# Kernel tuning notes

Hardware: AMD Instinct MI355X
Metric: run time of the kernel (lower is better)

Reference implementation:

```python
import jax, jax.numpy as jnp
import numpy as np

B, D, NTXT, H = 16384, 512, 4096, 1024


def _linear_params(key, fan_in, fan_out):
    kw, kb = jax.random.split(key)
    s = 1.0 / np.sqrt(fan_in)
    W = jax.random.uniform(kw, (fan_in, fan_out), jnp.float32, -s, s)
    b = jax.random.uniform(kb, (fan_out,), jnp.float32, -s, s)
    return W, b


def setup_inputs() -> dict:
    key = jax.random.key(0)
    ks = jax.random.split(key, 9)
    img_features = jax.random.normal(ks[0], (B, D), jnp.float32)
    txt_features = jax.random.normal(ks[1], (D, NTXT), jnp.float32)
    target_ind = jax.random.randint(ks[2], (B,), 0, NTXT, jnp.int32)
    Wi0, bi0 = _linear_params(ks[3], D, H)
    Wi1, bi1 = _linear_params(ks[4], H, H)
    Wi2, bi2 = _linear_params(ks[5], H, D)
    Wt0, bt0 = _linear_params(ks[6], D, H)
    Wt1, bt1 = _linear_params(ks[7], H, H)
    Wt2, bt2 = _linear_params(ks[8], H, D)
    logit_scale = jnp.asarray(np.log(1.0 / 0.07), jnp.float32)
    temp = jnp.asarray(1.0, jnp.float32)
    return {
        "img_features": img_features, "txt_features": txt_features,
        "target_ind": target_ind, "temp": temp,
        "Wi0": Wi0, "bi0": bi0, "Wi1": Wi1, "bi1": bi1, "Wi2": Wi2, "bi2": bi2,
        "Wt0": Wt0, "bt0": bt0, "Wt1": Wt1, "bt1": bt1, "Wt2": Wt2, "bt2": bt2,
        "logit_scale": logit_scale,
    }


def _mlp(x, params):
    # ReLU after every layer except the last (matches MLP.forward)
    for W, b in params[:-1]:
        x = jax.nn.relu(x @ W + b)
    W, b = params[-1]
    return x @ W + b


def reference(img_features, txt_features, target_ind, temp,
              Wi0, bi0, Wi1, bi1, Wi2, bi2,
              Wt0, bt0, Wt1, bt1, Wt2, bt2, logit_scale):
    p_img = _mlp(img_features, [(Wi0, bi0), (Wi1, bi1), (Wi2, bi2)])          # [B, D]
    p_txt = _mlp(txt_features.T, [(Wt0, bt0), (Wt1, bt1), (Wt2, bt2)])        # [N, D]

    sim = (p_img @ p_txt.T) * jnp.exp(logit_scale)                            # [B, N]
    sim = sim / jnp.linalg.norm(sim, axis=-1, keepdims=True)
    out_logits = sim / jnp.linalg.norm(sim, axis=-1, keepdims=True)           # faithful double-normalize

    # vectorized form of the per-sample Python-loop softmax-CE in MLP_CLIP_loss
    logp = jax.nn.log_softmax(out_logits / temp, axis=-1)                     # [B, N]
    picked = jnp.take_along_axis(logp, target_ind[:, None].astype(jnp.int32), axis=1)[:, 0]
    loss = -jnp.mean(picked)

    # accuracy branch (uses unscaled similarity, row-normalized)
    sim_clip = p_img @ p_txt.T
    sim_clip = sim_clip / jnp.linalg.norm(sim_clip, axis=-1, keepdims=True)
    acc = jnp.sum(jnp.argmax(sim_clip, axis=1).astype(jnp.int32) == target_ind)
    return loss, acc
```

## Files before the change

kernel.cpp:

```cpp
#include <hip/hip_runtime.h>
#include <cstdint>
#include <cstddef>

#define B_ROWS 16384
#define D_DIM  512
#define NTXT_N 4096
#define H_DIM  1024

typedef __attribute__((ext_vector_type(8))) short short8;
typedef __attribute__((ext_vector_type(4))) float f32x4;

__device__ __forceinline__ ushort f2bf(float x) {
    union { float f; uint32_t u; } c; c.f = x;
    const uint32_t u = c.u;
    return (ushort)((u + 0x7fffu + ((u >> 16) & 1u)) >> 16);
}
__device__ __forceinline__ float bf2f(ushort h) {
    union { uint32_t u; float f; } c; c.u = ((uint32_t)h) << 16;
    return c.f;
}

#define GLDS16(gp, lp) __builtin_amdgcn_global_load_lds( \
    (const __attribute__((address_space(1))) void*)(gp),  \
    (__attribute__((address_space(3))) void*)(lp), 16, 0, 0)

__device__ __forceinline__ void xcd_remap(int& bx, int& by) {
    const int nx = gridDim.x, ny = gridDim.y;
    const int nwg = nx * ny;
    const int bid = by * nx + bx;
    const int q = nwg >> 3, r = nwg & 7;
    const int xcd = bid & 7, idx = bid >> 3;
    const int nb = (xcd < r ? xcd * (q + 1) : r * (q + 1) + (xcd - r) * q) + idx;
    bx = nb % nx; by = nb / nx;
}

__global__ void init_kernel(int* acc) {
    if (threadIdx.x == 0 && blockIdx.x == 0) *acc = 0;
}

__global__ void tsplit_kernel(const float* __restrict__ in, ushort* __restrict__ oh,
                              ushort* __restrict__ ol, int R, int C, int cbase)
{
    __shared__ float tile[32][33];
    const int c0 = blockIdx.x * 32, r0 = blockIdx.y * 32;
    const int tx = threadIdx.x, ty = threadIdx.y;
    #pragma unroll
    for (int j = 0; j < 32; j += 8)
        tile[ty + j][tx] = in[(size_t)(r0 + ty + j) * C + cbase + c0 + tx];
    __syncthreads();
    #pragma unroll
    for (int j = 0; j < 32; j += 8) {
        const float v = tile[tx][ty + j];
        const ushort h = f2bf(v);
        const size_t idx = (size_t)(c0 + ty + j) * R + r0 + tx;
        oh[idx] = h;
        ol[idx] = f2bf(v - bf2f(h));
    }
}

__global__ void csplit_kernel(const float* __restrict__ in, ushort* __restrict__ oh,
                              ushort* __restrict__ ol, int n)
{
    const int i = (blockIdx.x * 256 + threadIdx.x) * 4;
    if (i >= n) return;
    const float4 f = *(const float4*)&in[i];
    ushort4 h, l;
    h.x = f2bf(f.x); l.x = f2bf(f.x - bf2f(h.x));
    h.y = f2bf(f.y); l.y = f2bf(f.y - bf2f(h.y));
    h.z = f2bf(f.z); l.z = f2bf(f.z - bf2f(h.z));
    h.w = f2bf(f.w); l.w = f2bf(f.w - bf2f(h.w));
    *(ushort4*)&oh[i] = h;
    *(ushort4*)&ol[i] = l;
}

template<int K, int OMODE, bool RELU, bool BIAS>
__global__ __launch_bounds__(256, 2)
void gemm_p2_kernel(const ushort* __restrict__ Ah, const ushort* __restrict__ Al,
                    const ushort* __restrict__ Bh, const ushort* __restrict__ Bl,
                    const float* __restrict__ bias,
                    float* __restrict__ Cf, ushort* __restrict__ Ch, ushort* __restrict__ Cl,
                    int M, int N)
{
    constexpr int NT = K / 32;
    __shared__ __align__(16) ushort LDSB[2 * 4 * 4096];

    const int tid  = threadIdx.x;
    const int lane = tid & 63;
    const int w    = tid >> 6;
    const int wr   = w >> 1, wc = w & 1;

    int bxi = blockIdx.x, byi = blockIdx.y;
    xcd_remap(bxi, byi);
    const int bm = byi * 128, bn = bxi * 128;

    const int    stlo  = w * 1024;
    const int    srow  = w * 32 + (lane >> 2);
    const int    scol  = (((lane & 3) ^ ((lane >> 3) & 3)) << 3);
    const size_t aoff0 = (size_t)(bm + srow) * K + scol;
    const size_t boff0 = (size_t)(bn + srow) * K + scol;

    const int frow = lane & 15;
    const int koff = ((lane >> 4) ^ ((frow >> 1) & 3)) << 3;

    f32x4 acc[4][4];
    #pragma unroll
    for (int m = 0; m < 4; ++m)
        #pragma unroll
        for (int n = 0; n < 4; ++n)
            acc[m][n] = (f32x4)0.0f;

#define STAGE(tt, bi) do {                                                    \
        const int _kk = (tt) * 32;                                            \
        ushort* _b = &LDSB[(bi) * 16384];                                     \
        GLDS16(Ah + aoff0 + _kk,          _b +         stlo);                 \
        GLDS16(Ah + aoff0 + _kk + 16 * K, _b +         stlo + 512);           \
        GLDS16(Al + aoff0 + _kk,          _b +  4096 + stlo);                 \
        GLDS16(Al + aoff0 + _kk + 16 * K, _b +  4096 + stlo + 512);           \
        GLDS16(Bh + boff0 + _kk,          _b +  8192 + stlo);                 \
        GLDS16(Bh + boff0 + _kk + 16 * K, _b +  8192 + stlo + 512);           \
        GLDS16(Bl + boff0 + _kk,          _b + 12288 + stlo);                 \
        GLDS16(Bl + boff0 + _kk + 16 * K, _b + 12288 + stlo + 512);           \
    } while (0)

#define COMPUTE(bi) do {                                                      \
        const ushort* _Ahs = &LDSB[(bi) * 16384];                             \
        const ushort* _Als = _Ahs + 4096;                                     \
        const ushort* _Bhs = _Ahs + 8192;                                     \
        const ushort* _Bls = _Ahs + 12288;                                    \
        short8 a_h[4], a_l[4], b_h[4], b_l[4];                                \
        _Pragma("unroll")                                                     \
        for (int m = 0; m < 4; ++m) {                                         \
            const int off = (wr * 64 + m * 16 + frow) * 32 + koff;            \
            a_h[m] = *(const short8*)&_Ahs[off];                              \
            a_l[m] = *(const short8*)&_Als[off];                              \
        }                                                                     \
        _Pragma("unroll")                                                     \
        for (int n = 0; n < 4; ++n) {                                         \
            const int off = (wc * 64 + n * 16 + frow) * 32 + koff;            \
            b_h[n] = *(const short8*)&_Bhs[off];                              \
            b_l[n] = *(const short8*)&_Bls[off];                              \
        }                                                                     \
        __builtin_amdgcn_s_setprio(1);                                        \
        _Pragma("unroll")                                                     \
        for (int m = 0; m < 4; ++m)                                           \
            _Pragma("unroll")                                                 \
            for (int n = 0; n < 4; ++n) {                                     \
                acc[m][n] = __builtin_amdgcn_mfma_f32_16x16x32_bf16(          \
                    a_h[m], b_h[n], acc[m][n], 0, 0, 0);                      \
                acc[m][n] = __builtin_amdgcn_mfma_f32_16x16x32_bf16(          \
                    a_h[m], b_l[n], acc[m][n], 0, 0, 0);                      \
                acc[m][n] = __builtin_amdgcn_mfma_f32_16x16x32_bf16(          \
                    a_l[m], b_h[n], acc[m][n], 0, 0, 0);                      \
            }                                                                 \
        __builtin_amdgcn_s_setprio(0);                                        \
    } while (0)

    STAGE(0, 0);
    #pragma unroll 2
    for (int t = 0; t < NT; ++t) {
        __syncthreads();
        if (t + 1 < NT) STAGE(t + 1, (t + 1) & 1);
        COMPUTE(t & 1);
    }

#undef STAGE
#undef COMPUTE

    const int crow0 = bm + wr * 64 + (lane >> 4) * 4;
    const int ccol0 = bn + wc * 64 + (lane & 15);
    #pragma unroll
    for (int m = 0; m < 4; ++m)
        #pragma unroll
        for (int n = 0; n < 4; ++n) {
            const int col = ccol0 + n * 16;
            const float bv = BIAS ? bias[col] : 0.0f;
            #pragma unroll
            for (int q = 0; q < 4; ++q) {
                float v = acc[m][n][q] + bv;
                if (RELU) v = fmaxf(v, 0.0f);
                const size_t idx = (size_t)(crow0 + m * 16 + q) * N + col;
                if (OMODE == 0) {
                    Cf[idx] = v;
                } else {
                    const ushort h = f2bf(v);
                    Ch[idx] = h;
                    Cl[idx] = f2bf(v - bf2f(h));
                }
            }
        }
}

template<int K, int OMODE, bool RELU, bool BIAS>
__global__ __launch_bounds__(512, 2)
void gemm256_kernel(const ushort* __restrict__ Ah, const ushort* __restrict__ Al,
                    const ushort* __restrict__ Bh, const ushort* __restrict__ Bl,
                    const float* __restrict__ bias,
                    float* __restrict__ Cf, ushort* __restrict__ Ch, ushort* __restrict__ Cl,
                    int M, int N)
{
    constexpr int NT = K / 32;
    __shared__ __align__(16) ushort LDSB[2 * 4 * 8192];

    const int tid  = threadIdx.x;
    const int lane = tid & 63;
    const int w    = tid >> 6;
    const int wr   = w >> 2, wc = w & 3;

    int bxi = blockIdx.x, byi = blockIdx.y;
    xcd_remap(bxi, byi);
    const int bm = byi * 256, bn = bxi * 256;

    const int    srow  = tid >> 2;
    const int    scol  = (((tid & 3) ^ ((tid >> 3) & 3)) << 3);
    const size_t aoffA = (size_t)(bm + srow) * K + scol;
    const size_t aoffB = (size_t)(bm + 128 + srow) * K + scol;
    const size_t boffA = (size_t)(bn + srow) * K + scol;
    const size_t boffB = (size_t)(bn + 128 + srow) * K + scol;
    const int    dst   = srow * 32 + (tid & 3) * 8;

    const int frow = lane & 15;
    const int koff = ((lane >> 4) ^ ((frow >> 1) & 3)) << 3;

    f32x4 acc[8][4];
    #pragma unroll
    for (int m = 0; m < 8; ++m)
        #pragma unroll
        for (int n = 0; n < 4; ++n)
            acc[m][n] = (f32x4)0.0f;

#define STAGE256(tt, bi) do {                                                 \
        const int _kk = (tt) * 32;                                            \
        ushort* _b = &LDSB[(bi) * 32768];                                     \
        GLDS16(Ah + aoffA + _kk, _b +         dst);                           \
        GLDS16(Ah + aoffB + _kk, _b +         dst + 4096);                    \
        GLDS16(Al + aoffA + _kk, _b +  8192 + dst);                           \
        GLDS16(Al + aoffB + _kk, _b +  8192 + dst + 4096);                    \
        GLDS16(Bh + boffA + _kk, _b + 16384 + dst);                           \
        GLDS16(Bh + boffB + _kk, _b + 16384 + dst + 4096);                    \
        GLDS16(Bl + boffA + _kk, _b + 24576 + dst);                           \
        GLDS16(Bl + boffB + _kk, _b + 24576 + dst + 4096);                    \
    } while (0)

#define COMPUTE256(bi) do {                                                   \
        const ushort* _Ahs = &LDSB[(bi) * 32768];                             \
        const ushort* _Als = _Ahs + 8192;                                     \
        const ushort* _Bhs = _Ahs + 16384;                                    \
        const ushort* _Bls = _Ahs + 24576;                                    \
        short8 b_h[4], b_l[4];                                                \
        _Pragma("unroll")                                                     \
        for (int n = 0; n < 4; ++n) {                                         \
            const int off = (wc * 64 + n * 16 + frow) * 32 + koff;            \
            b_h[n] = *(const short8*)&_Bhs[off];                              \
            b_l[n] = *(const short8*)&_Bls[off];                              \
        }                                                                     \
        __builtin_amdgcn_s_setprio(1);                                        \
        _Pragma("unroll")                                                     \
        for (int m = 0; m < 8; ++m) {                                         \
            const int off = (wr * 128 + m * 16 + frow) * 32 + koff;           \
            const short8 a_h = *(const short8*)&_Ahs[off];                    \
            const short8 a_l = *(const short8*)&_Als[off];                    \
            _Pragma("unroll")                                                 \
            for (int n = 0; n < 4; ++n) {                                     \
                acc[m][n] = __builtin_amdgcn_mfma_f32_16x16x32_bf16(          \
                    a_h, b_h[n], acc[m][n], 0, 0, 0);                         \
                acc[m][n] = __builtin_amdgcn_mfma_f32_16x16x32_bf16(          \
                    a_h, b_l[n], acc[m][n], 0, 0, 0);                         \
                acc[m][n] = __builtin_amdgcn_mfma_f32_16x16x32_bf16(          \
                    a_l, b_h[n], acc[m][n], 0, 0, 0);                         \
            }                                                                 \
        }                                                                     \
        __builtin_amdgcn_s_setprio(0);                                        \
    } while (0)

    STAGE256(0, 0);
    #pragma unroll 2
    for (int t = 0; t < NT; ++t) {
        __syncthreads();
        if (t + 1 < NT) STAGE256(t + 1, (t + 1) & 1);
        COMPUTE256(t & 1);
    }

#undef STAGE256
#undef COMPUTE256

    const int crow0 = bm + wr * 128 + (lane >> 4) * 4;
    const int ccol0 = bn + wc * 64 + (lane & 15);
    #pragma unroll
    for (int m = 0; m < 8; ++m)
        #pragma unroll
        for (int n = 0; n < 4; ++n) {
            const int col = ccol0 + n * 16;
            const float bv = BIAS ? bias[col] : 0.0f;
            #pragma unroll
            for (int q = 0; q < 4; ++q) {
                float v = acc[m][n][q] + bv;
                if (RELU) v = fmaxf(v, 0.0f);
                const size_t idx = (size_t)(crow0 + m * 16 + q) * N + col;
                if (OMODE == 0) {
                    Cf[idx] = v;
                } else {
                    const ushort h = f2bf(v);
                    Ch[idx] = h;
                    Cl[idx] = f2bf(v - bf2f(h));
                }
            }
        }
}

__global__ __launch_bounds__(256) void rowreduce_kernel(
    const float* __restrict__ sim, const int* __restrict__ tgt,
    const float* __restrict__ temp_p, float* __restrict__ perrow,
    int* __restrict__ acc_cnt, int row0)
{
    const int row = blockIdx.x;
    const float* srow = sim + (size_t)row * NTXT_N;
    const int tid = threadIdx.x;

    float v[16];
    #pragma unroll
    for (int q = 0; q < 4; ++q) {
        float4 f = *(const float4*)&srow[4 * tid + 1024 * q];
        v[4 * q + 0] = f.x; v[4 * q + 1] = f.y; v[4 * q + 2] = f.z; v[4 * q + 3] = f.w;
    }

    float ss = 0.0f, mx = -3.4e38f; int mi = 0x7fffffff;
    #pragma unroll
    for (int q = 0; q < 4; ++q)
        #pragma unroll
        for (int r = 0; r < 4; ++r) {
            const int j = 4 * tid + 1024 * q + r;
            const float x = v[4 * q + r];
            ss = fmaf(x, x, ss);
            if (x > mx) { mx = x; mi = j; }
            else if (x == mx && j < mi) mi = j;
        }

    #pragma unroll
    for (int off = 32; off; off >>= 1) {
        ss += __shfl_down(ss, off);
        const float omx = __shfl_down(mx, off);
        const int   omi = __shfl_down(mi, off);
        if (omx > mx || (omx == mx && omi < mi)) { mx = omx; mi = omi; }
    }

    __shared__ float sws[4], swm[4];
    __shared__ int   swi[4];
    __shared__ float bC, bMx;
    __shared__ int   bAmax;
    const int w = tid >> 6, lane = tid & 63;
    if (lane == 0) { sws[w] = ss; swm[w] = mx; swi[w] = mi; }
    __syncthreads();
    if (tid == 0) {
        float tss = 0.0f, tmx = -3.4e38f; int tmi = 0x7fffffff;
        #pragma unroll
        for (int i = 0; i < 4; ++i) {
            tss += sws[i];
            if (swm[i] > tmx || (swm[i] == tmx && swi[i] < tmi)) { tmx = swm[i]; tmi = swi[i]; }
        }
        const float inv_nr = 1.0f / sqrtf(tss);
        const float n2 = sqrtf(tss * inv_nr * inv_nr);
        const float Cv = inv_nr / (n2 * temp_p[0]);
        bC = Cv; bMx = tmx * Cv; bAmax = tmi;
    }
    __syncthreads();
    const float Cv = bC, mxx = bMx;

    float es = 0.0f;
    #pragma unroll
    for (int q = 0; q < 16; ++q) es += expf(v[q] * Cv - mxx);
    #pragma unroll
    for (int off = 32; off; off >>= 1) es += __shfl_down(es, off);
    if (lane == 0) sws[w] = es;
    __syncthreads();
    if (tid == 0) {
        const float tes = sws[0] + sws[1] + sws[2] + sws[3];
        const float lse = mxx + logf(tes);
        const int t = tgt[row0 + row];
        perrow[row0 + row] = lse - srow[t] * Cv;
        if (bAmax == t) atomicAdd(acc_cnt, 1);
    }
}

__global__ __launch_bounds__(256) void finalize_kernel(
    const float* __restrict__ perrow, const int* __restrict__ acc_cnt,
    float* __restrict__ out)
{
    __shared__ float red[256];
    const int tid = threadIdx.x;
    float s = 0.0f;
    for (int i = tid; i < B_ROWS; i += 256) s += perrow[i];
    red[tid] = s;
    __syncthreads();
    for (int st = 128; st; st >>= 1) {
        if (tid < st) red[tid] += red[tid + st];
        __syncthreads();
    }
    if (tid == 0) {
        out[0] = red[0] / (float)B_ROWS;
        out[1] = (float)(*acc_cnt);
    }
}

extern "C" void kernel_launch(void* const* d_in, const int* in_sizes, int n_in,
                              void* d_out, int out_size, void* d_ws, size_t ws_size,
                              hipStream_t stream)
{
    const float* img  = (const float*)d_in[0];
    const float* txt  = (const float*)d_in[1];
    const int*   tgt  = (const int*)  d_in[2];
    const float* temp = (const float*)d_in[3];
    const float* Wf[6] = { (const float*)d_in[4],  (const float*)d_in[6],  (const float*)d_in[8],
                           (const float*)d_in[10], (const float*)d_in[12], (const float*)d_in[14] };
    const float* bf[6] = { (const float*)d_in[5],  (const float*)d_in[7],  (const float*)d_in[9],
                           (const float*)d_in[11], (const float*)d_in[13], (const float*)d_in[15] };
    float* out = (float*)d_out;

    const int wK[6] = { D_DIM, H_DIM, H_DIM, D_DIM, H_DIM, H_DIM };
    const int wN[6] = { H_DIM, H_DIM, D_DIM, H_DIM, H_DIM, D_DIM };

    auto need = [&](size_t ch, size_t sc) -> size_t {
        size_t wt = 0;
        for (int i = 0; i < 6; ++i) wt += (size_t)wK[i] * wN[i] * 2 * 2;
        const size_t a01 = 2 * (ch * H_DIM * 2 * 2);
        const size_t pt  = (size_t)NTXT_N * D_DIM * 2 * 2;
        const size_t sim = sc * NTXT_N * 4;
        return wt + a01 + pt + sim + (size_t)B_ROWS * 4 + (size_t)64 * 1024;
    };
    const size_t ladder[][2] = { {16384, 4096}, {16384, 2048}, {8192, 4096}, {8192, 2048},
                                 {4096, 2048},  {4096, 1024},  {2048, 1024}, {1024, 1024} };
    size_t CH = 1024, SIMCH = 512;
    for (auto& e : ladder)
        if (need(e[0], e[1]) <= ws_size) { CH = e[0]; SIMCH = e[1]; break; }

    uint8_t* p = (uint8_t*)d_ws;
    auto alloc = [&](size_t bytes) -> void* {
        void* r = (void*)p; p += (bytes + 255) & ~(size_t)255; return r;
    };
    ushort* WTh[6]; ushort* WTl[6];
    for (int i = 0; i < 6; ++i) {
        WTh[i] = (ushort*)alloc((size_t)wK[i] * wN[i] * 2);
        WTl[i] = (ushort*)alloc((size_t)wK[i] * wN[i] * 2);
    }
    ushort* A0h = (ushort*)alloc(CH * H_DIM * 2);
    ushort* A0l = (ushort*)alloc(CH * H_DIM * 2);
    ushort* A1h = (ushort*)alloc(CH * H_DIM * 2);
    ushort* A1l = (ushort*)alloc(CH * H_DIM * 2);
    ushort* PTh = (ushort*)alloc((size_t)NTXT_N * D_DIM * 2);
    ushort* PTl = (ushort*)alloc((size_t)NTXT_N * D_DIM * 2);
    float*  SIM = (float*)alloc(SIMCH * NTXT_N * 4);
    float*  PERROW = (float*)alloc((size_t)B_ROWS * 4);
    int*    ACC = (int*)alloc(64);
    ushort* XBh = A1h;  ushort* XBl = A1l;
    ushort* PIh = A0h;  ushort* PIl = A0l;

    init_kernel<<<1, 64, 0, stream>>>(ACC);

    for (int i = 0; i < 6; ++i)
        tsplit_kernel<<<dim3(wN[i] / 32, wK[i] / 32), dim3(32, 8), 0, stream>>>(
            Wf[i], WTh[i], WTl[i], wK[i], wN[i], 0);

    const size_t CHT = CH < (size_t)NTXT_N ? CH : (size_t)NTXT_N;
    for (size_t n0 = 0; n0 < NTXT_N; n0 += CHT) {
        tsplit_kernel<<<dim3(CHT / 32, D_DIM / 32), dim3(32, 8), 0, stream>>>(
            txt, XBh, XBl, D_DIM, NTXT_N, (int)n0);
        gemm_p2_kernel<D_DIM, 1, true, true><<<dim3(H_DIM / 128, CHT / 128), 256, 0, stream>>>(
            XBh, XBl, WTh[3], WTl[3], bf[3], nullptr, A0h, A0l, (int)CHT, H_DIM);
        gemm_p2_kernel<H_DIM, 1, true, true><<<dim3(H_DIM / 128, CHT / 128), 256, 0, stream>>>(
            A0h, A0l, WTh[4], WTl[4], bf[4], nullptr, A1h, A1l, (int)CHT, H_DIM);
        gemm_p2_kernel<H_DIM, 1, false, true><<<dim3(D_DIM / 128, CHT / 128), 256, 0, stream>>>(
            A1h, A1l, WTh[5], WTl[5], bf[5], nullptr,
            PTh + n0 * D_DIM, PTl + n0 * D_DIM, (int)CHT, D_DIM);
    }

    const bool big = (CH % 256 == 0) && (CH >= 4096);
    for (size_t m0 = 0; m0 < B_ROWS; m0 += CH) {
        csplit_kernel<<<(CH * D_DIM / 4 + 255) / 256, 256, 0, stream>>>(
            img + m0 * D_DIM, XBh, XBl, (int)(CH * D_DIM));
        if (big) {
            gemm256_kernel<D_DIM, 1, true, true><<<dim3(H_DIM / 256, CH / 256), 512, 0, stream>>>(
                XBh, XBl, WTh[0], WTl[0], bf[0], nullptr, A0h, A0l, (int)CH, H_DIM);
            gemm256_kernel<H_DIM, 1, true, true><<<dim3(H_DIM / 256, CH / 256), 512, 0, stream>>>(
                A0h, A0l, WTh[1], WTl[1], bf[1], nullptr, A1h, A1l, (int)CH, H_DIM);
        } else {
            gemm_p2_kernel<D_DIM, 1, true, true><<<dim3(H_DIM / 128, CH / 128), 256, 0, stream>>>(
                XBh, XBl, WTh[0], WTl[0], bf[0], nullptr, A0h, A0l, (int)CH, H_DIM);
            gemm_p2_kernel<H_DIM, 1, true, true><<<dim3(H_DIM / 128, CH / 128), 256, 0, stream>>>(
                A0h, A0l, WTh[1], WTl[1], bf[1], nullptr, A1h, A1l, (int)CH, H_DIM);
        }
        gemm_p2_kernel<H_DIM, 1, false, true><<<dim3(D_DIM / 128, CH / 128), 256, 0, stream>>>(
            A1h, A1l, WTh[2], WTl[2], bf[2], nullptr, PIh, PIl, (int)CH, D_DIM);
        for (size_t s0 = 0; s0 < CH; s0 += SIMCH) {
            if ((SIMCH % 256 == 0) && SIMCH >= 2048) {
                gemm256_kernel<D_DIM, 0, false, false><<<dim3(NTXT_N / 256, SIMCH / 256), 512, 0, stream>>>(
                    PIh + s0 * D_DIM, PIl + s0 * D_DIM, PTh, PTl, nullptr,
                    SIM, nullptr, nullptr, (int)SIMCH, NTXT_N);
            } else {
                gemm_p2_kernel<D_DIM, 0, false, false><<<dim3(NTXT_N / 128, SIMCH / 128), 256, 0, stream>>>(
                    PIh + s0 * D_DIM, PIl + s0 * D_DIM, PTh, PTl, nullptr,
                    SIM, nullptr, nullptr, (int)SIMCH, NTXT_N);
            }
            rowreduce_kernel<<<SIMCH, 256, 0, stream>>>(
                SIM, tgt, temp, PERROW, ACC, (int)(m0 + s0));
        }
    }

    finalize_kernel<<<1, 256, 0, stream>>>(PERROW, ACC, out);
}
```

Baseline: 659.7 us.

## Pipeline 256-tile GEMM with 5-slot rotating LDS ring and split A/B prefetch

Replaces the double-buffered stage/compute loop of the 256x256 split-bf16 GEMM with a five-slot LDS ring in which the A and B halves of each K-step occupy separate slots. Loads are issued at staggered points: B for the next step before the compute, and A two steps ahead midway through the MFMA work. Each iteration uses explicit vmcnt waits and one raw barrier. The aim is to keep more global-to-LDS traffic in flight and hide load latency behind MFMAs. In exchange it uses more LDS (160 KB, which may limit the two-blocks-per-CU target) and relies on hand-counted waitcnt values being correct.

```diff
diff --git a/kernel.cpp b/kernel.cpp
--- a/kernel.cpp
+++ b/kernel.cpp
@@ -199,7 +199,7 @@
                     int M, int N)
 {
     constexpr int NT = K / 32;
-    __shared__ __align__(16) ushort LDSB[2 * 4 * 8192];
+    __shared__ __align__(16) ushort LDSB[5 * 16384];
 
     const int tid  = threadIdx.x;
     const int lane = tid & 63;
@@ -228,60 +228,85 @@
         for (int n = 0; n < 4; ++n)
             acc[m][n] = (f32x4)0.0f;
 
-#define STAGE256(tt, bi) do {                                                 \
+#define ISSUE_A(tt) do {                                                      \
         const int _kk = (tt) * 32;                                            \
-        ushort* _b = &LDSB[(bi) * 32768];                                     \
-        GLDS16(Ah + aoffA + _kk, _b +         dst);                           \
-        GLDS16(Ah + aoffB + _kk, _b +         dst + 4096);                    \
-        GLDS16(Al + aoffA + _kk, _b +  8192 + dst);                           \
-        GLDS16(Al + aoffB + _kk, _b +  8192 + dst + 4096);                    \
-        GLDS16(Bh + boffA + _kk, _b + 16384 + dst);                           \
-        GLDS16(Bh + boffB + _kk, _b + 16384 + dst + 4096);                    \
-        GLDS16(Bl + boffA + _kk, _b + 24576 + dst);                           \
-        GLDS16(Bl + boffB + _kk, _b + 24576 + dst + 4096);                    \
+        ushort* _b = &LDSB[((2 * (tt)) % 5) * 16384];                         \
+        GLDS16(Ah + aoffA + _kk, _b + dst);                                   \
+        GLDS16(Ah + aoffB + _kk, _b + dst + 4096);                            \
+        GLDS16(Al + aoffA + _kk, _b + 8192 + dst);                            \
+        GLDS16(Al + aoffB + _kk, _b + 8192 + dst + 4096);                     \
     } while (0)
 
-#define COMPUTE256(bi) do {                                                   \
-        const ushort* _Ahs = &LDSB[(bi) * 32768];                             \
-        const ushort* _Als = _Ahs + 8192;                                     \
-        const ushort* _Bhs = _Ahs + 16384;                                    \
-        const ushort* _Bls = _Ahs + 24576;                                    \
-        short8 b_h[4], b_l[4];                                                \
-        _Pragma("unroll")                                                     \
-        for (int n = 0; n < 4; ++n) {                                         \
-            const int off = (wc * 64 + n * 16 + frow) * 32 + koff;            \
-            b_h[n] = *(const short8*)&_Bhs[off];                              \
-            b_l[n] = *(const short8*)&_Bls[off];                              \
-        }                                                                     \
-        __builtin_amdgcn_s_setprio(1);                                        \
-        _Pragma("unroll")                                                     \
-        for (int m = 0; m < 8; ++m) {                                         \
-            const int off = (wr * 128 + m * 16 + frow) * 32 + koff;           \
-            const short8 a_h = *(const short8*)&_Ahs[off];                    \
-            const short8 a_l = *(const short8*)&_Als[off];                    \
-            _Pragma("unroll")                                                 \
-            for (int n = 0; n < 4; ++n) {                                     \
-                acc[m][n] = __builtin_amdgcn_mfma_f32_16x16x32_bf16(          \
-                    a_h, b_h[n], acc[m][n], 0, 0, 0);                         \
-                acc[m][n] = __builtin_amdgcn_mfma_f32_16x16x32_bf16(          \
-                    a_h, b_l[n], acc[m][n], 0, 0, 0);                         \
-                acc[m][n] = __builtin_amdgcn_mfma_f32_16x16x32_bf16(          \
-                    a_l, b_h[n], acc[m][n], 0, 0, 0);                         \
-            }                                                                 \
-        }                                                                     \
-        __builtin_amdgcn_s_setprio(0);                                        \
+#define ISSUE_B(tt) do {                                                      \
+        const int _kk = (tt) * 32;                                            \
+        ushort* _b = &LDSB[((2 * (tt) + 1) % 5) * 16384];                     \
+        GLDS16(Bh + boffA + _kk, _b + dst);                                   \
+        GLDS16(Bh + boffB + _kk, _b + dst + 4096);                            \
+        GLDS16(Bl + boffA + _kk, _b + 8192 + dst);                            \
+        GLDS16(Bl + boffB + _kk, _b + 8192 + dst + 4096);                     \
     } while (0)
 
-    STAGE256(0, 0);
-    #pragma unroll 2
+    ISSUE_A(0);
+    ISSUE_B(0);
+    if (NT > 1) ISSUE_A(1);
+
     for (int t = 0; t < NT; ++t) {
-        __syncthreads();
-        if (t + 1 < NT) STAGE256(t + 1, (t + 1) & 1);
-        COMPUTE256(t & 1);
-    }
-
-#undef STAGE256
-#undef COMPUTE256
+        if (t < NT - 1) {
+            asm volatile("s_waitcnt lgkmcnt(0)\n\ts_waitcnt vmcnt(4)" ::: "memory");
+        } else {
+            asm volatile("s_waitcnt lgkmcnt(0)\n\ts_waitcnt vmcnt(0)" ::: "memory");
+        }
+        __builtin_amdgcn_s_barrier();
+        __builtin_amdgcn_sched_barrier(0);
+
+        if (t + 1 < NT) ISSUE_B(t + 1);
+
+        const ushort* aU = &LDSB[((2 * t) % 5) * 16384];
+        const ushort* bU = &LDSB[((2 * t + 1) % 5) * 16384];
+
+        short8 b_h[4], b_l[4];
+        #pragma unroll
+        for (int n = 0; n < 4; ++n) {
+            const int off = (wc * 64 + n * 16 + frow) * 32 + koff;
+            b_h[n] = *(const short8*)&bU[off];
+            b_l[n] = *(const short8*)&bU[8192 + off];
+        }
+
+        __builtin_amdgcn_s_setprio(1);
+        #pragma unroll
+        for (int m = 0; m < 4; ++m) {
+            const int off = (wr * 128 + m * 16 + frow) * 32 + koff;
+            const short8 a_h = *(const short8*)&aU[off];
+            const short8 a_l = *(const short8*)&aU[8192 + off];
+            #pragma unroll
+            for (int n = 0; n < 4; ++n) {
+                acc[m][n] = __builtin_amdgcn_mfma_f32_16x16x32_bf16(a_h, b_h[n], acc[m][n], 0, 0, 0);
+                acc[m][n] = __builtin_amdgcn_mfma_f32_16x16x32_bf16(a_h, b_l[n], acc[m][n], 0, 0, 0);
+                acc[m][n] = __builtin_amdgcn_mfma_f32_16x16x32_bf16(a_l, b_h[n], acc[m][n], 0, 0, 0);
+            }
+        }
+        __builtin_amdgcn_s_setprio(0);
+
+        if (t + 2 < NT) ISSUE_A(t + 2);
+
+        __builtin_amdgcn_s_setprio(1);
+        #pragma unroll
+        for (int m = 4; m < 8; ++m) {
+            const int off = (wr * 128 + m * 16 + frow) * 32 + koff;
+            const short8 a_h = *(const short8*)&aU[off];
+            const short8 a_l = *(const short8*)&aU[8192 + off];
+            #pragma unroll
+            for (int n = 0; n < 4; ++n) {
+                acc[m][n] = __builtin_amdgcn_mfma_f32_16x16x32_bf16(a_h, b_h[n], acc[m][n], 0, 0, 0);
+                acc[m][n] = __builtin_amdgcn_mfma_f32_16x16x32_bf16(a_h, b_l[n], acc[m][n], 0, 0, 0);
+                acc[m][n] = __builtin_amdgcn_mfma_f32_16x16x32_bf16(a_l, b_h[n], acc[m][n], 0, 0, 0);
+            }
+        }
+        __builtin_amdgcn_s_setprio(0);
+    }
+
+#undef ISSUE_A
+#undef ISSUE_B
 
     const int crow0 = bm + wr * 128 + (lane >> 4) * 4;
     const int ccol0 = bn + wc * 64 + (lane & 15);
```

Measured after the change: 684.8 us. 1.04x slower.

## Split MFMA main loop into four barrier-synchronized phases with explicit waitcnts

Applied to the files above, without the earlier changes.

Restructures the 256-tile bf16x3 GEMM inner loop so that A fragments are loaded from LDS in four quarter-phases interleaved with MFMA bursts. Explicit s_barrier and waitcnt instructions replace __syncthreads, so the global-to-LDS prefetch for the next tile is issued early and only waited on at the end of the iteration. The goal is to overlap LDS reads with MFMA work and keep waves in lockstep. It also adds a larger sim-chunk rung to the workspace ladder, allowing bigger similarity chunks when workspace permits. The extra barriers could add synchronization overhead.

```diff
diff --git a/kernel.cpp b/kernel.cpp
--- a/kernel.cpp
+++ b/kernel.cpp
@@ -241,47 +241,77 @@
         GLDS16(Bl + boffB + _kk, _b + 24576 + dst + 4096);                    \
     } while (0)
 
-#define COMPUTE256(bi) do {                                                   \
-        const ushort* _Ahs = &LDSB[(bi) * 32768];                             \
-        const ushort* _Als = _Ahs + 8192;                                     \
-        const ushort* _Bhs = _Ahs + 16384;                                    \
-        const ushort* _Bls = _Ahs + 24576;                                    \
-        short8 b_h[4], b_l[4];                                                \
+#define LOADA(q) do {                                                         \
+        const int _o0 = (wr * 128 + (2 * (q)) * 16 + frow) * 32 + koff;       \
+        a_h0 = *(const short8*)&aU[_o0];                                      \
+        a_l0 = *(const short8*)&aU[8192 + _o0];                               \
+        a_h1 = *(const short8*)&aU[_o0 + 512];                                \
+        a_l1 = *(const short8*)&aU[8192 + _o0 + 512];                         \
+    } while (0)
+
+#define MFMAQ(q) do {                                                         \
+        __builtin_amdgcn_s_setprio(1);                                        \
         _Pragma("unroll")                                                     \
         for (int n = 0; n < 4; ++n) {                                         \
-            const int off = (wc * 64 + n * 16 + frow) * 32 + koff;            \
-            b_h[n] = *(const short8*)&_Bhs[off];                              \
-            b_l[n] = *(const short8*)&_Bls[off];                              \
-        }                                                                     \
-        __builtin_amdgcn_s_setprio(1);                                        \
-        _Pragma("unroll")                                                     \
-        for (int m = 0; m < 8; ++m) {                                         \
-            const int off = (wr * 128 + m * 16 + frow) * 32 + koff;           \
-            const short8 a_h = *(const short8*)&_Ahs[off];                    \
-            const short8 a_l = *(const short8*)&_Als[off];                    \
-            _Pragma("unroll")                                                 \
-            for (int n = 0; n < 4; ++n) {                                     \
-                acc[m][n] = __builtin_amdgcn_mfma_f32_16x16x32_bf16(          \
-                    a_h, b_h[n], acc[m][n], 0, 0, 0);                         \
-                acc[m][n] = __builtin_amdgcn_mfma_f32_16x16x32_bf16(          \
-                    a_h, b_l[n], acc[m][n], 0, 0, 0);                         \
-                acc[m][n] = __builtin_amdgcn_mfma_f32_16x16x32_bf16(          \
-                    a_l, b_h[n], acc[m][n], 0, 0, 0);                         \
-            }                                                                 \
+            acc[2*(q)][n]   = __builtin_amdgcn_mfma_f32_16x16x32_bf16(a_h0, b_h[n], acc[2*(q)][n],   0, 0, 0); \
+            acc[2*(q)][n]   = __builtin_amdgcn_mfma_f32_16x16x32_bf16(a_h0, b_l[n], acc[2*(q)][n],   0, 0, 0); \
+            acc[2*(q)][n]   = __builtin_amdgcn_mfma_f32_16x16x32_bf16(a_l0, b_h[n], acc[2*(q)][n],   0, 0, 0); \
+            acc[2*(q)+1][n] = __builtin_amdgcn_mfma_f32_16x16x32_bf16(a_h1, b_h[n], acc[2*(q)+1][n], 0, 0, 0); \
+            acc[2*(q)+1][n] = __builtin_amdgcn_mfma_f32_16x16x32_bf16(a_h1, b_l[n], acc[2*(q)+1][n], 0, 0, 0); \
+            acc[2*(q)+1][n] = __builtin_amdgcn_mfma_f32_16x16x32_bf16(a_l1, b_h[n], acc[2*(q)+1][n], 0, 0, 0); \
         }                                                                     \
         __builtin_amdgcn_s_setprio(0);                                        \
     } while (0)
 
     STAGE256(0, 0);
-    #pragma unroll 2
+    asm volatile("s_waitcnt vmcnt(0)" ::: "memory");
+    __builtin_amdgcn_s_barrier();
+
     for (int t = 0; t < NT; ++t) {
-        __syncthreads();
-        if (t + 1 < NT) STAGE256(t + 1, (t + 1) & 1);
-        COMPUTE256(t & 1);
+        const int bi = t & 1;
+        const ushort* aU = &LDSB[bi * 32768];
+        const ushort* bU = aU + 16384;
+
+        short8 b_h[4], b_l[4];
+        short8 a_h0, a_l0, a_h1, a_l1;
+
+        #pragma unroll
+        for (int n = 0; n < 4; ++n) {
+            const int off = (wc * 64 + n * 16 + frow) * 32 + koff;
+            b_h[n] = *(const short8*)&bU[off];
+            b_l[n] = *(const short8*)&bU[8192 + off];
+        }
+        LOADA(0);
+        if (t + 1 < NT) STAGE256(t + 1, bi ^ 1);
+        __builtin_amdgcn_s_barrier();
+        asm volatile("s_waitcnt lgkmcnt(0)" ::: "memory");
+        MFMAQ(0);
+        __builtin_amdgcn_s_barrier();
+
+        LOADA(1);
+        __builtin_amdgcn_s_barrier();
+        asm volatile("s_waitcnt lgkmcnt(0)" ::: "memory");
+        MFMAQ(1);
+        __builtin_amdgcn_s_barrier();
+
+        LOADA(2);
+        __builtin_amdgcn_s_barrier();
+        asm volatile("s_waitcnt lgkmcnt(0)" ::: "memory");
+        MFMAQ(2);
+        __builtin_amdgcn_s_barrier();
+
+        LOADA(3);
+        __builtin_amdgcn_s_barrier();
+        asm volatile("s_waitcnt lgkmcnt(0)" ::: "memory");
+        MFMAQ(3);
+        if (t + 1 < NT)
+            asm volatile("s_waitcnt vmcnt(0)" ::: "memory");
+        __builtin_amdgcn_s_barrier();
     }
 
 #undef STAGE256
-#undef COMPUTE256
+#undef LOADA
+#undef MFMAQ
 
     const int crow0 = bm + wr * 128 + (lane >> 4) * 4;
     const int ccol0 = bn + wc * 64 + (lane & 15);
@@ -426,7 +456,8 @@
         const size_t sim = sc * NTXT_N * 4;
         return wt + a01 + pt + sim + (size_t)B_ROWS * 4 + (size_t)64 * 1024;
     };
-    const size_t ladder[][2] = { {16384, 4096}, {16384, 2048}, {8192, 4096}, {8192, 2048},
+    const size_t ladder[][2] = { {16384, 8192}, {16384, 4096}, {16384, 2048},
+                                 {8192, 4096},  {8192, 2048},
                                  {4096, 2048},  {4096, 1024},  {2048, 1024}, {1024, 1024} };
     size_t CH = 1024, SIMCH = 512;
     for (auto& e : ladder)
```

New measurement: 715.4 us. 8.4% more time.
